# Performance work log

Measured on AMD Instinct MI355X. Metric: run time of the kernel, lower is better.

Reference implementation:

```python
import jax, jax.numpy as jnp
import numpy as np

NUM_HEADS = 16
CHUNK = 64
RMS_EPS = 1.1920928955078125e-07  # torch.finfo(float32).eps, F.rms_norm default


def setup_inputs() -> dict:
    key = jax.random.key(0)
    k1, k2, k3 = jax.random.split(key, 3)
    B, S, D = 2, 4096, 2048
    x = jax.random.normal(k1, (B, S, D), dtype=jnp.float32)
    w_in = jax.random.normal(k2, (5 * D, D), dtype=jnp.float32) * 0.02
    w_out = jax.random.normal(k3, (D, D), dtype=jnp.float32) * 0.02
    return {"x": x, "w_in": w_in, "w_out": w_out}


def _forward(x, w_in, w_out):
    B, S, D = x.shape
    H, hd, C = NUM_HEADS, D // NUM_HEADS, CHUNK
    proj = x @ w_in.T                              # [B,S,5D]
    q, k, v, a, g = jnp.split(proj, 5, axis=-1)
    rs = lambda t: t.reshape(B, S, H, hd)
    q, k, v, a, g = map(rs, (q, k, v, a, g))
    # rms_norm over head_dim, no learned weight
    q = q * jax.lax.rsqrt(jnp.mean(q * q, axis=-1, keepdims=True) + RMS_EPS)
    k = jnp.tanh(k)
    a = jnp.clip(jax.nn.sigmoid(a + 2.0), 0.6, 0.9995)
    u = k * v                                      # updates, float32
    NC = S // C
    # [NC, B, C, H, hd] so lax.scan iterates over chunks
    a_r = a.reshape(B, NC, C, H, hd).transpose(1, 0, 2, 3, 4)
    u_r = u.reshape(B, NC, C, H, hd).transpose(1, 0, 2, 3, 4)

    def step(state, au):
        a_c, u_c = au                              # [B,C,H,hd]
        prefix = jnp.cumprod(a_c, axis=1)
        acc = jnp.cumsum(u_c / jnp.maximum(prefix, 1e-6), axis=1)
        states = prefix * (state[:, None] + acc)   # [B,C,H,hd]
        return states[:, -1], states

    state0 = jnp.zeros((B, H, hd), dtype=jnp.float32)
    _, mem = jax.lax.scan(step, state0, (a_r, u_r))  # [NC,B,C,H,hd]
    memory = mem.transpose(1, 0, 2, 3, 4).reshape(B, S, H, hd)
    gate = jax.nn.sigmoid(g)
    y = gate * (q * memory) + (1.0 - gate) * v
    return y.reshape(B, S, D) @ w_out.T


def reference(x, w_in, w_out):
    return _forward(x, w_in, w_out)
```

## Files before the change

kernel.cpp:

```cpp
#include <hip/hip_runtime.h>
#include <cstdint>
#include <cstddef>

typedef unsigned short u16;
typedef __bf16 bf16x8 __attribute__((ext_vector_type(8)));
typedef float f32x16 __attribute__((ext_vector_type(16)));
typedef unsigned int u32;
typedef u32 u32x4 __attribute__((ext_vector_type(4)));
typedef float f32x4v __attribute__((ext_vector_type(4)));

#define BB 2
#define SS 4096
#define DD 2048
#define HH 16
#define HD 128
#define CC 64
#define NC 64
#define D5 10240
#define RMS_EPS 1.1920928955078125e-07f

__device__ __forceinline__ u16 f2bf(float f) {
  uint32_t x = __float_as_uint(f);
  uint32_t r = (x + 0x7fffu + ((x >> 16) & 1u)) >> 16;
  return (u16)r;
}
__device__ __forceinline__ float bf2f(u16 u) {
  return __uint_as_float(((uint32_t)u) << 16);
}
__device__ __forceinline__ float fast_sigmoid(float x) {
  return 1.0f / (1.0f + __expf(-x));
}
__device__ __forceinline__ float fast_tanh(float x) {
  return 1.0f - 2.0f / (__expf(2.0f * x) + 1.0f);
}

__global__ void cvt_bf16x8_kernel(const f32x4v* __restrict__ src,
                                  u32x4* __restrict__ dst, int n8) {
  int i = blockIdx.x * blockDim.x + threadIdx.x;
  int stride = gridDim.x * blockDim.x;
  for (; i < n8; i += stride) {
    f32x4v a = src[2 * i];
    f32x4v b = src[2 * i + 1];
    u32x4 o;
    o.x = (u32)f2bf(a.x) | ((u32)f2bf(a.y) << 16);
    o.y = (u32)f2bf(a.z) | ((u32)f2bf(a.w) << 16);
    o.z = (u32)f2bf(b.x) | ((u32)f2bf(b.y) << 16);
    o.w = (u32)f2bf(b.z) | ((u32)f2bf(b.w) << 16);
    dst[i] = o;
  }
}

template <typename OutT>
__global__ __launch_bounds__(256) void gemm_bt(const u16* __restrict__ A,
                                               const u16* __restrict__ B,
                                               OutT* __restrict__ C,
                                               int M, int N, int K) {
  __shared__ u16 As[128 * 32];
  __shared__ u16 Bs[128 * 32];

  const int tid = threadIdx.x;
  const int wave = tid >> 6;
  const int lane = tid & 63;
  const int m0 = blockIdx.x * 128;
  const int n0 = blockIdx.y * 128;
  const int wm = (wave & 1) * 64;
  const int wn = (wave >> 1) * 64;

  f32x16 acc[2][2] = {};

  const int srow = wave * 32 + (lane >> 2);
  const int scol = ((lane & 3) ^ ((lane >> 3) & 3)) * 8;
  const u16* Ag0 = A + (size_t)(m0 + srow) * K + scol;
  const u16* Ag1 = A + (size_t)(m0 + srow + 16) * K + scol;
  const u16* Bg0 = B + (size_t)(n0 + srow) * K + scol;
  const u16* Bg1 = B + (size_t)(n0 + srow + 16) * K + scol;
  u16* Al0 = &As[(wave * 32) * 32];
  u16* Al1 = &As[(wave * 32 + 16) * 32];
  u16* Bl0 = &Bs[(wave * 32) * 32];
  u16* Bl1 = &Bs[(wave * 32 + 16) * 32];

  const int fr = lane & 31;
  const int fc = lane >> 5;
  const int fx = (lane >> 1) & 3;

  for (int k0 = 0; k0 < K; k0 += 32) {
    __builtin_amdgcn_global_load_lds(
        (__attribute__((address_space(1))) void*)(u16*)(Ag0 + k0),
        (__attribute__((address_space(3))) void*)Al0, 16, 0, 0);
    __builtin_amdgcn_global_load_lds(
        (__attribute__((address_space(1))) void*)(u16*)(Ag1 + k0),
        (__attribute__((address_space(3))) void*)Al1, 16, 0, 0);
    __builtin_amdgcn_global_load_lds(
        (__attribute__((address_space(1))) void*)(u16*)(Bg0 + k0),
        (__attribute__((address_space(3))) void*)Bl0, 16, 0, 0);
    __builtin_amdgcn_global_load_lds(
        (__attribute__((address_space(1))) void*)(u16*)(Bg1 + k0),
        (__attribute__((address_space(3))) void*)Bl1, 16, 0, 0);
    __syncthreads();

    bf16x8 af[2][2], bfg[2][2];
#pragma unroll
    for (int ks = 0; ks < 2; ++ks) {
      const int pc = ((ks * 2 + fc) ^ fx) * 8;
#pragma unroll
      for (int mt = 0; mt < 2; ++mt)
        af[mt][ks] = *(const bf16x8*)&As[(wm + mt * 32 + fr) * 32 + pc];
#pragma unroll
      for (int nt = 0; nt < 2; ++nt)
        bfg[nt][ks] = *(const bf16x8*)&Bs[(wn + nt * 32 + fr) * 32 + pc];
    }

#pragma unroll
    for (int ks = 0; ks < 2; ++ks)
#pragma unroll
      for (int mt = 0; mt < 2; ++mt)
#pragma unroll
        for (int nt = 0; nt < 2; ++nt)
          acc[mt][nt] = __builtin_amdgcn_mfma_f32_32x32x16_bf16(
              af[mt][ks], bfg[nt][ks], acc[mt][nt], 0, 0, 0);

    __syncthreads();
  }

  const int ccol = lane & 31;
  const int rbase = 4 * (lane >> 5);
#pragma unroll
  for (int mt = 0; mt < 2; ++mt) {
#pragma unroll
    for (int nt = 0; nt < 2; ++nt) {
      const size_t cb = (size_t)(n0 + wn + nt * 32 + ccol);
      const size_t rb = (size_t)(m0 + wm + mt * 32 + rbase);
#pragma unroll
      for (int reg = 0; reg < 16; ++reg) {
        const int r = (reg & 3) + 8 * (reg >> 2);
        OutT* Cp = C + (rb + r) * N + cb;
        if constexpr (sizeof(OutT) == 2)
          *Cp = (OutT)f2bf(acc[mt][nt][reg]);
        else
          *Cp = acc[mt][nt][reg];
      }
    }
  }
}

__global__ __launch_bounds__(64) void scan_chunk(const u16* __restrict__ proj,
                                                 float* __restrict__ Pc,
                                                 float* __restrict__ Lc) {
  const int idx = blockIdx.x;
  const int h = idx & (HH - 1);
  const int c = (idx >> 4) & (NC - 1);
  const int b = idx >> 10;
  const int lane = threadIdx.x;

  const size_t row0 = (size_t)(b * SS + c * CC) * D5 + h * HD;

  float p0 = 1.0f, a0 = 0.0f, p1 = 1.0f, a1 = 0.0f;
  for (int t = 0; t < CC; ++t) {
    const size_t rp = row0 + (size_t)t * D5;
    float k0 = bf2f(proj[rp + DD + lane]);
    float k1 = bf2f(proj[rp + DD + lane + 64]);
    float v0 = bf2f(proj[rp + 2 * DD + lane]);
    float v1 = bf2f(proj[rp + 2 * DD + lane + 64]);
    float ar0 = bf2f(proj[rp + 3 * DD + lane]);
    float ar1 = bf2f(proj[rp + 3 * DD + lane + 64]);
    float aa0 = fminf(fmaxf(fast_sigmoid(ar0 + 2.0f), 0.6f), 0.9995f);
    float aa1 = fminf(fmaxf(fast_sigmoid(ar1 + 2.0f), 0.6f), 0.9995f);
    p0 *= aa0;
    p1 *= aa1;
    a0 += fast_tanh(k0) * v0 / fmaxf(p0, 1e-6f);
    a1 += fast_tanh(k1) * v1 / fmaxf(p1, 1e-6f);
  }
  const size_t ci = ((size_t)(b * NC + c) * HH + h) * HD;
  Pc[ci + lane] = p0;
  Pc[ci + lane + 64] = p1;
  Lc[ci + lane] = p0 * a0;
  Lc[ci + lane + 64] = p1 * a1;
}

__global__ void scan_carry(const float* __restrict__ Pc, const float* __restrict__ Lc,
                           float* __restrict__ Sin) {
  const int t = blockIdx.x * blockDim.x + threadIdx.x;
  const int b = t >> 11;
  const int hd = t & (DD - 1);
  float state = 0.0f;
  for (int c = 0; c < NC; ++c) {
    const size_t i = (size_t)(b * NC + c) * DD + hd;
    Sin[i] = state;
    state = Pc[i] * state + Lc[i];
  }
}

__global__ __launch_bounds__(64) void finalize_y(const u16* __restrict__ proj,
                                                 const float* __restrict__ Sin,
                                                 u16* __restrict__ y) {
  const int idx = blockIdx.x;
  const int h = idx & (HH - 1);
  const int c = (idx >> 4) & (NC - 1);
  const int b = idx >> 10;
  const int lane = threadIdx.x;

  const size_t row0 = (size_t)(b * SS + c * CC) * D5 + h * HD;
  const size_t out0 = (size_t)(b * SS + c * CC) * DD + h * HD;
  const size_t sinb = (size_t)(b * NC + c) * DD + h * HD;
  const float sin0 = Sin[sinb + lane];
  const float sin1 = Sin[sinb + lane + 64];

  float p0 = 1.0f, a0 = 0.0f, p1 = 1.0f, a1 = 0.0f;
  for (int t = 0; t < CC; ++t) {
    const size_t rp = row0 + (size_t)t * D5;
    const float q0 = bf2f(proj[rp + lane]);
    const float q1 = bf2f(proj[rp + lane + 64]);
    const float k0 = bf2f(proj[rp + DD + lane]);
    const float k1 = bf2f(proj[rp + DD + lane + 64]);
    const float v0 = bf2f(proj[rp + 2 * DD + lane]);
    const float v1 = bf2f(proj[rp + 2 * DD + lane + 64]);
    const float ar0 = bf2f(proj[rp + 3 * DD + lane]);
    const float ar1 = bf2f(proj[rp + 3 * DD + lane + 64]);
    const float g0 = bf2f(proj[rp + 4 * DD + lane]);
    const float g1 = bf2f(proj[rp + 4 * DD + lane + 64]);

    const float aa0 = fminf(fmaxf(fast_sigmoid(ar0 + 2.0f), 0.6f), 0.9995f);
    const float aa1 = fminf(fmaxf(fast_sigmoid(ar1 + 2.0f), 0.6f), 0.9995f);
    p0 *= aa0;
    p1 *= aa1;
    a0 += fast_tanh(k0) * v0 / fmaxf(p0, 1e-6f);
    a1 += fast_tanh(k1) * v1 / fmaxf(p1, 1e-6f);
    const float mem0 = p0 * (sin0 + a0);
    const float mem1 = p1 * (sin1 + a1);

    float ss = q0 * q0 + q1 * q1;
#pragma unroll
    for (int m = 32; m; m >>= 1) ss += __shfl_xor(ss, m);
    const float rn = rsqrtf(ss * (1.0f / 128.0f) + RMS_EPS);

    const float gt0 = fast_sigmoid(g0);
    const float gt1 = fast_sigmoid(g1);
    y[out0 + (size_t)t * DD + lane] = f2bf(gt0 * (q0 * rn * mem0) + (1.0f - gt0) * v0);
    y[out0 + (size_t)t * DD + lane + 64] = f2bf(gt1 * (q1 * rn * mem1) + (1.0f - gt1) * v1);
  }
}

extern "C" void kernel_launch(void* const* d_in, const int* in_sizes, int n_in,
                              void* d_out, int out_size, void* d_ws, size_t ws_size,
                              hipStream_t stream) {
  const float* x = (const float*)d_in[0];
  const float* w_in = (const float*)d_in[1];
  const float* w_out = (const float*)d_in[2];
  float* out = (float*)d_out;

  char* ws = (char*)d_ws;
  size_t off = 0;
  auto alloc = [&](size_t bytes) -> void* {
    void* p = ws + off;
    off += (bytes + 255) & ~(size_t)255;
    return p;
  };
  const size_t nBS = (size_t)BB * SS;
  u16* projb = (u16*)alloc(nBS * D5 * 2);
  u16* xb    = (u16*)alloc(nBS * DD * 2);
  u16* wib   = (u16*)alloc((size_t)D5 * DD * 2);
  u16* wob   = (u16*)alloc((size_t)DD * DD * 2);
  float* Pc  = (float*)alloc((size_t)BB * NC * DD * 4);
  float* Lc  = (float*)alloc((size_t)BB * NC * DD * 4);
  float* Sin = (float*)alloc((size_t)BB * NC * DD * 4);
  u16* yb = xb;
  (void)in_sizes; (void)n_in; (void)out_size;

  if (off > ws_size) return;

  cvt_bf16x8_kernel<<<1024, 256, 0, stream>>>((const f32x4v*)x, (u32x4*)xb,
                                              (int)(nBS * DD / 8));
  cvt_bf16x8_kernel<<<1024, 256, 0, stream>>>((const f32x4v*)w_in, (u32x4*)wib,
                                              (int)((size_t)D5 * DD / 8));
  cvt_bf16x8_kernel<<<1024, 256, 0, stream>>>((const f32x4v*)w_out, (u32x4*)wob,
                                              (int)((size_t)DD * DD / 8));

  gemm_bt<u16><<<dim3(64, 80), 256, 0, stream>>>(xb, wib, projb, 8192, 10240, 2048);

  scan_chunk<<<BB * NC * HH, 64, 0, stream>>>(projb, Pc, Lc);

  scan_carry<<<16, 256, 0, stream>>>(Pc, Lc, Sin);

  finalize_y<<<BB * NC * HH, 64, 0, stream>>>(projb, Sin, yb);

  gemm_bt<float><<<dim3(64, 16), 256, 0, stream>>>(yb, wob, out, 8192, 2048, 2048);
}
```

Baseline: 776.6 us.

## Rewrite GEMM with 256x256 tiles, double-buffered LDS pipeline and block swizzle

```diff
diff --git a/kernel.cpp b/kernel.cpp
--- a/kernel.cpp
+++ b/kernel.cpp
@@ -4,7 +4,6 @@
 
 typedef unsigned short u16;
 typedef __bf16 bf16x8 __attribute__((ext_vector_type(8)));
-typedef float f32x16 __attribute__((ext_vector_type(16)));
 typedef unsigned int u32;
 typedef u32 u32x4 __attribute__((ext_vector_type(4)));
 typedef float f32x4v __attribute__((ext_vector_type(4)));
@@ -51,96 +50,170 @@
 }
 
 template <typename OutT>
-__global__ __launch_bounds__(256) void gemm_bt(const u16* __restrict__ A,
-                                               const u16* __restrict__ B,
-                                               OutT* __restrict__ C,
-                                               int M, int N, int K) {
-  __shared__ u16 As[128 * 32];
-  __shared__ u16 Bs[128 * 32];
+__global__ __launch_bounds__(512, 2) void gemm_bt(const u16* __restrict__ A,
+                                                  const u16* __restrict__ B,
+                                                  OutT* __restrict__ C,
+                                                  int M, int N, int K) {
+  __shared__ u16 lds[65536];
 
   const int tid = threadIdx.x;
   const int wave = tid >> 6;
   const int lane = tid & 63;
-  const int m0 = blockIdx.x * 128;
-  const int n0 = blockIdx.y * 128;
-  const int wm = (wave & 1) * 64;
-  const int wn = (wave >> 1) * 64;
-
-  f32x16 acc[2][2] = {};
-
-  const int srow = wave * 32 + (lane >> 2);
-  const int scol = ((lane & 3) ^ ((lane >> 3) & 3)) * 8;
-  const u16* Ag0 = A + (size_t)(m0 + srow) * K + scol;
-  const u16* Ag1 = A + (size_t)(m0 + srow + 16) * K + scol;
-  const u16* Bg0 = B + (size_t)(n0 + srow) * K + scol;
-  const u16* Bg1 = B + (size_t)(n0 + srow + 16) * K + scol;
-  u16* Al0 = &As[(wave * 32) * 32];
-  u16* Al1 = &As[(wave * 32 + 16) * 32];
-  u16* Bl0 = &Bs[(wave * 32) * 32];
-  u16* Bl1 = &Bs[(wave * 32 + 16) * 32];
-
-  const int fr = lane & 31;
-  const int fc = lane >> 5;
-  const int fx = (lane >> 1) & 3;
-
-  for (int k0 = 0; k0 < K; k0 += 32) {
-    __builtin_amdgcn_global_load_lds(
-        (__attribute__((address_space(1))) void*)(u16*)(Ag0 + k0),
-        (__attribute__((address_space(3))) void*)Al0, 16, 0, 0);
-    __builtin_amdgcn_global_load_lds(
-        (__attribute__((address_space(1))) void*)(u16*)(Ag1 + k0),
-        (__attribute__((address_space(3))) void*)Al1, 16, 0, 0);
-    __builtin_amdgcn_global_load_lds(
-        (__attribute__((address_space(1))) void*)(u16*)(Bg0 + k0),
-        (__attribute__((address_space(3))) void*)Bl0, 16, 0, 0);
-    __builtin_amdgcn_global_load_lds(
-        (__attribute__((address_space(1))) void*)(u16*)(Bg1 + k0),
-        (__attribute__((address_space(3))) void*)Bl1, 16, 0, 0);
-    __syncthreads();
-
-    bf16x8 af[2][2], bfg[2][2];
+
+  const int nwg = (int)gridDim.x;
+  const int bid = (int)blockIdx.x;
+  const int bswz = (bid & 7) * (nwg >> 3) + (bid >> 3);
+  const int Mt = M >> 8;
+  const int m0 = (bswz % Mt) << 8;
+  const int n0 = (bswz / Mt) << 8;
+
+  const int wm = (wave >> 2) << 7;
+  const int wn = (wave & 3) << 6;
+
+  const int s_r = tid >> 3;
+  const int s_ls = (tid & 7) ^ (s_r & 7);
+  const u16* Ast = A + (size_t)(m0 + s_r) * K + s_ls * 8;
+  const u16* Bst = B + (size_t)(n0 + s_r) * K + s_ls * 8;
+  const int s_lb = wave * 512;
+
+  const int fr = lane & 15;
+  const int fg = lane >> 4;
+  const int fx = lane & 7;
+  const int psk0 = ((0 + fg) ^ fx) * 8;
+  const int psk1 = ((4 + fg) ^ fx) * 8;
+  const int aro = (wm + fr) * 64;
+  const int bro = 16384 + (wn + fr) * 64;
+
+  f32x4v acc[8][4] = {};
+  bf16x8 afr[4][2];
+  bf16x8 bfr[2][2][2];
+  const int NT = K >> 6;
+
+#define BARF()                              \
+  do {                                      \
+    asm volatile("" ::: "memory");          \
+    __builtin_amdgcn_s_barrier();           \
+    asm volatile("" ::: "memory");          \
+  } while (0)
+
+#define STAGE(GB, LB, H, KT)                                                    \
+  do {                                                                          \
+    const u16* g_ = (GB) + (size_t)((H) * 128) * K + (KT) * 64;                 \
+    __builtin_amdgcn_global_load_lds(                                           \
+        (__attribute__((address_space(1))) void*)(u16*)g_,                      \
+        (__attribute__((address_space(3))) void*)&lds[(LB) + (H) * 8192 + s_lb],\
+        16, 0, 0);                                                              \
+    __builtin_amdgcn_global_load_lds(                                           \
+        (__attribute__((address_space(1))) void*)(u16*)(g_ + (size_t)64 * K),   \
+        (__attribute__((address_space(3))) void*)&lds[(LB) + (H) * 8192 + 4096 + s_lb], \
+        16, 0, 0);                                                              \
+  } while (0)
+
+#define LOADA(BO, MH)                                             \
+  do {                                                            \
+    _Pragma("unroll") for (int mf = 0; mf < 4; ++mf) {            \
+      const int ab_ = (BO) + aro + (MH) * 4096 + mf * 1024;       \
+      afr[mf][0] = *(const bf16x8*)&lds[ab_ + psk0];              \
+      afr[mf][1] = *(const bf16x8*)&lds[ab_ + psk1];              \
+    }                                                             \
+  } while (0)
+
+#define LOADB(BO, NH)                                             \
+  do {                                                            \
+    _Pragma("unroll") for (int nf = 0; nf < 2; ++nf) {            \
+      const int bb_ = (BO) + bro + (NH) * 2048 + nf * 1024;       \
+      bfr[NH][nf][0] = *(const bf16x8*)&lds[bb_ + psk0];          \
+      bfr[NH][nf][1] = *(const bf16x8*)&lds[bb_ + psk1];          \
+    }                                                             \
+  } while (0)
+
+#define MMAQ(MH, NH)                                                          \
+  do {                                                                        \
+    __builtin_amdgcn_s_setprio(1);                                            \
+    _Pragma("unroll") for (int mf = 0; mf < 4; ++mf)                          \
+        _Pragma("unroll") for (int nf = 0; nf < 2; ++nf) {                    \
+      acc[(MH) * 4 + mf][(NH) * 2 + nf] =                                     \
+          __builtin_amdgcn_mfma_f32_16x16x32_bf16(                            \
+              afr[mf][0], bfr[NH][nf][0], acc[(MH) * 4 + mf][(NH) * 2 + nf],  \
+              0, 0, 0);                                                       \
+      acc[(MH) * 4 + mf][(NH) * 2 + nf] =                                     \
+          __builtin_amdgcn_mfma_f32_16x16x32_bf16(                            \
+              afr[mf][1], bfr[NH][nf][1], acc[(MH) * 4 + mf][(NH) * 2 + nf],  \
+              0, 0, 0);                                                       \
+    }                                                                         \
+    __builtin_amdgcn_s_setprio(0);                                            \
+    __builtin_amdgcn_sched_barrier(0);                                        \
+  } while (0)
+
+  STAGE(Ast, 0, 0, 0);
+  STAGE(Ast, 0, 1, 0);
+  STAGE(Bst, 16384, 0, 0);
+  STAGE(Bst, 16384, 1, 0);
+  {
+    const int k1 = (NT > 1) ? 1 : 0;
+    STAGE(Ast, 32768, 0, k1);
+    STAGE(Ast, 32768, 1, k1);
+    STAGE(Bst, 49152, 0, k1);
+    STAGE(Bst, 49152, 1, k1);
+  }
+  asm volatile("s_waitcnt vmcnt(8)" ::: "memory");
+  BARF();
+
+  for (int t = 0; t < NT; ++t) {
+    const int bo = (t & 1) << 15;
+    const int t2 = (t + 2 < NT) ? t + 2 : NT - 1;
+
+    LOADA(bo, 0);
+    LOADB(bo, 0);
+    BARF();
+    MMAQ(0, 0);
+    BARF();
+
+    LOADB(bo, 1);
+    BARF();
+    MMAQ(0, 1);
+    BARF();
+
+    LOADA(bo, 1);
+    BARF();
+    MMAQ(1, 1);
+    BARF();
+
+    STAGE(Ast, bo, 0, t2);
+    STAGE(Bst, bo + 16384, 0, t2);
+    STAGE(Ast, bo, 1, t2);
+    STAGE(Bst, bo + 16384, 1, t2);
+    BARF();
+    MMAQ(1, 0);
+    asm volatile("s_waitcnt vmcnt(8)" ::: "memory");
+    BARF();
+  }
+
+  asm volatile("s_waitcnt vmcnt(0)" ::: "memory");
+
+  const int ccol = lane & 15;
+  const int crow = (lane >> 4) << 2;
 #pragma unroll
-    for (int ks = 0; ks < 2; ++ks) {
-      const int pc = ((ks * 2 + fc) ^ fx) * 8;
+  for (int am = 0; am < 8; ++am) {
+    const size_t r0 = (size_t)(m0 + wm + ((am >> 2) << 6) + ((am & 3) << 4) + crow);
 #pragma unroll
-      for (int mt = 0; mt < 2; ++mt)
-        af[mt][ks] = *(const bf16x8*)&As[(wm + mt * 32 + fr) * 32 + pc];
+    for (int an = 0; an < 4; ++an) {
+      const size_t c0 = (size_t)(n0 + wn + ((an >> 1) << 5) + ((an & 1) << 4) + ccol);
 #pragma unroll
-      for (int nt = 0; nt < 2; ++nt)
-        bfg[nt][ks] = *(const bf16x8*)&Bs[(wn + nt * 32 + fr) * 32 + pc];
-    }
-
-#pragma unroll
-    for (int ks = 0; ks < 2; ++ks)
-#pragma unroll
-      for (int mt = 0; mt < 2; ++mt)
-#pragma unroll
-        for (int nt = 0; nt < 2; ++nt)
-          acc[mt][nt] = __builtin_amdgcn_mfma_f32_32x32x16_bf16(
-              af[mt][ks], bfg[nt][ks], acc[mt][nt], 0, 0, 0);
-
-    __syncthreads();
-  }
-
-  const int ccol = lane & 31;
-  const int rbase = 4 * (lane >> 5);
-#pragma unroll
-  for (int mt = 0; mt < 2; ++mt) {
-#pragma unroll
-    for (int nt = 0; nt < 2; ++nt) {
-      const size_t cb = (size_t)(n0 + wn + nt * 32 + ccol);
-      const size_t rb = (size_t)(m0 + wm + mt * 32 + rbase);
-#pragma unroll
-      for (int reg = 0; reg < 16; ++reg) {
-        const int r = (reg & 3) + 8 * (reg >> 2);
-        OutT* Cp = C + (rb + r) * N + cb;
+      for (int r = 0; r < 4; ++r) {
+        OutT* Cp = C + (r0 + r) * (size_t)N + c0;
         if constexpr (sizeof(OutT) == 2)
-          *Cp = (OutT)f2bf(acc[mt][nt][reg]);
+          *Cp = (OutT)f2bf(acc[am][an][r]);
         else
-          *Cp = acc[mt][nt][reg];
+          *Cp = acc[am][an][r];
       }
     }
   }
+#undef BARF
+#undef STAGE
+#undef LOADA
+#undef LOADB
+#undef MMAQ
 }
 
 __global__ __launch_bounds__(64) void scan_chunk(const u16* __restrict__ proj,
@@ -275,7 +348,7 @@
   cvt_bf16x8_kernel<<<1024, 256, 0, stream>>>((const f32x4v*)w_out, (u32x4*)wob,
                                               (int)((size_t)DD * DD / 8));
 
-  gemm_bt<u16><<<dim3(64, 80), 256, 0, stream>>>(xb, wib, projb, 8192, 10240, 2048);
+  gemm_bt<u16><<<dim3(32 * 40), 512, 0, stream>>>(xb, wib, projb, 8192, 10240, 2048);
 
   scan_chunk<<<BB * NC * HH, 64, 0, stream>>>(projb, Pc, Lc);
 
@@ -283,5 +356,5 @@
 
   finalize_y<<<BB * NC * HH, 64, 0, stream>>>(projb, Sin, yb);
 
-  gemm_bt<float><<<dim3(64, 16), 256, 0, stream>>>(yb, wob, out, 8192, 2048, 2048);
-}
+  gemm_bt<float><<<dim3(32 * 8), 512, 0, stream>>>(yb, wob, out, 8192, 2048, 2048);
+}
```

Result: faster. 690.7 us (-11.1%).
